# Optimization experiments

Measured on AMD Instinct MI355X. Metric: run time of the kernel, lower is better.

## Reference

```python
import jax, jax.numpy as jnp
import numpy as np
from jax import lax

B, L, C = 4, 4096, 512
H = 8           # head_num
D = C // H      # head dim = 64
RR = 4          # reduction_ratio -> reducer conv kernel 7, stride 4
KS = 3          # MixFFN depthwise kernel
ER = 4          # expansion ratio -> 2048 channels
EPS = 1e-5      # torch LayerNorm default eps


def _ln(x, g, b):
    # LayerNorm over last axis, affine per-channel
    m = jnp.mean(x, axis=-1, keepdims=True)
    v = jnp.mean(jnp.square(x - m), axis=-1, keepdims=True)
    return (x - m) * lax.rsqrt(v + EPS) * g + b


def setup_inputs() -> dict:
    key = jax.random.key(0)
    ks = jax.random.split(key, 9)
    s = lambda fan: 1.0 / np.sqrt(fan)
    return {
        "x": jax.random.normal(ks[0], (B, L, C), jnp.float32),
        "w_q": jax.random.normal(ks[1], (C, C), jnp.float32) * s(C),
        "w_k": jax.random.normal(ks[2], (C, C), jnp.float32) * s(C),
        "w_v": jax.random.normal(ks[3], (C, C), jnp.float32) * s(C),
        "w_o": jax.random.normal(ks[4], (C, C), jnp.float32) * s(C),
        "w_red": jax.random.normal(ks[5], (C, C, 2 * RR - 1), jnp.float32) * s(C * (2 * RR - 1)),
        "w_ffn1": jax.random.normal(ks[6], (C, C), jnp.float32) * s(C),
        "w_ffn_dw": jax.random.normal(ks[7], (C * ER, 1, KS), jnp.float32) * s(KS),
        "w_ffn2": jax.random.normal(ks[8], (C, C * ER), jnp.float32) * s(C * ER),
        "ln_gamma": jnp.ones((6, C), jnp.float32),
        "ln_beta": jnp.zeros((6, C), jnp.float32),
    }


def reference(x, w_q, w_k, w_v, w_o, w_red, w_ffn1, w_ffn_dw, w_ffn2, ln_gamma, ln_beta):
    # ln indices: 0=ln1(pre-attn), 1=ln(reducer), 2=ln_q, 3=ln_k, 4=ln_v, 5=ln2(pre-ffn)
    residual = x
    h = _ln(x, ln_gamma[0], ln_beta[0])  # B L C

    # --- spatial-reduction for K/V: reflect-pad strided conv + LN ---
    p = (2 * RR - 1) // 2
    hr = jnp.transpose(h, (0, 2, 1))  # B C L
    hr = jnp.pad(hr, ((0, 0), (0, 0), (p, p)), mode="reflect")
    red = lax.conv_general_dilated(hr, w_red, window_strides=(RR,), padding="VALID",
                                   dimension_numbers=("NCH", "OIH", "NCH"))  # B C Lr
    red = jnp.transpose(red, (0, 2, 1))  # B Lr C
    red = _ln(red, ln_gamma[1], ln_beta[1])

    # --- QKV projections + LayerNorms ---
    q = _ln(h @ w_q.T, ln_gamma[2], ln_beta[2])      # B L C
    k = _ln(red @ w_k.T, ln_gamma[3], ln_beta[3])    # B Lr C
    v = _ln(red @ w_v.T, ln_gamma[4], ln_beta[4])    # B Lr C

    Lr = k.shape[1]
    q = q.reshape(B, L, H, D).transpose(0, 2, 1, 3)   # B h L d
    k = k.reshape(B, Lr, H, D).transpose(0, 2, 1, 3)  # B h Lr d
    v = v.reshape(B, Lr, H, D).transpose(0, 2, 1, 3)

    scores = jnp.einsum("bhqd,bhkd->bhqk", q, k) / jnp.sqrt(jnp.float32(D))
    attn = jax.nn.softmax(scores, axis=-1)
    out = jnp.einsum("bhqk,bhkd->bhqd", attn, v)
    out = out.transpose(0, 2, 1, 3).reshape(B, L, C)
    out = out @ w_o.T

    h2 = out + residual
    residual2 = h2
    f = _ln(h2, ln_gamma[5], ln_beta[5])  # B L C

    # --- MixFFN: 1x1 conv -> depthwise reflect conv (groups=C, out=ER*C) -> GELU -> 1x1 conv ---
    f = jnp.transpose(f, (0, 2, 1))  # B C L
    f = jnp.einsum("oi,bil->bol", w_ffn1, f)  # 1x1, C->C
    pk = (KS - 1) // 2
    fp = jnp.pad(f, ((0, 0), (0, 0), (pk, pk)), mode="reflect")
    f = lax.conv_general_dilated(fp, w_ffn_dw, window_strides=(1,), padding="VALID",
                                 dimension_numbers=("NCH", "OIH", "NCH"),
                                 feature_group_count=C)  # B (ER*C) L
    f = jax.nn.gelu(f, approximate=False)  # torch nn.GELU() is exact erf
    f = jnp.einsum("oi,bil->bol", w_ffn2, f)  # 1x1, ER*C->C
    f = jnp.transpose(f, (0, 2, 1))  # B L C

    return f + residual2
```

## Files before the change

kernel.cpp:

```cpp
#include <hip/hip_runtime.h>
#include <math.h>

typedef __attribute__((ext_vector_type(8))) short short8;
typedef __attribute__((ext_vector_type(4))) short short4v;
typedef __attribute__((ext_vector_type(4))) float f32x4;
typedef unsigned short u16;
typedef unsigned int u32;
typedef unsigned long long u64;

namespace {
constexpr int kB = 4;
constexpr int kL = 4096;
constexpr int kC = 512;
constexpr int kH = 8;
constexpr int kLr = 1024;
constexpr int kCH = 2048;
constexpr int kKred = 3584;
constexpr float kEps = 1e-5f;
}

#if __has_builtin(__builtin_amdgcn_mfma_f32_16x16x16bf16_1k)
#define MFMA16X16(a, b, c) __builtin_amdgcn_mfma_f32_16x16x16bf16_1k((a), (b), (c), 0, 0, 0)
#else
__device__ __forceinline__ f32x4 mfma16_fb(short4v a, short4v b, f32x4 c) {
  asm volatile("v_mfma_f32_16x16x16_bf16 %0, %1, %2, %0\n\ts_nop 7\n\ts_nop 3"
               : "+v"(c) : "v"(a), "v"(b));
  return c;
}
#define MFMA16X16(a, b, c) mfma16_fb((a), (b), (c))
#endif

__device__ __forceinline__ float bf2f(u16 u) { return __uint_as_float(((u32)u) << 16); }
__device__ __forceinline__ u16 f2bf(float f) {
  u32 u = __float_as_uint(f);
  u32 r = (u + 0x7fffu + ((u >> 16) & 1u)) >> 16;
  return (u16)r;
}
__device__ __forceinline__ u32 cvtpk(float lo, float hi) {
  u32 r;
  asm("v_cvt_pk_bf16_f32 %0, %1, %2" : "=v"(r) : "v"(lo), "v"(hi));
  return r;
}
__device__ __forceinline__ float fexp2(float x) {
#if __has_builtin(__builtin_amdgcn_exp2f)
  return __builtin_amdgcn_exp2f(x);
#else
  float r;
  asm("v_exp_f32 %0, %1" : "=v"(r) : "v"(x));
  return r;
#endif
}

__device__ __forceinline__ void gload_lds16(const void* g, void* l) {
  __builtin_amdgcn_global_load_lds(
      (const __attribute__((address_space(1))) unsigned int*)g,
      (__attribute__((address_space(3))) unsigned int*)l, 16, 0, 0);
}

__device__ __forceinline__ short8 ldsfrag(const u16* base, int row, int col16) {
  return *(const short8*)(base + (size_t)(((row << 3) + (col16 ^ (row & 7))) << 3));
}

__global__ __launch_bounds__(256) void cvt_weights_kernel(
    const float* __restrict__ w_q, const float* __restrict__ w_k,
    const float* __restrict__ w_v, const float* __restrict__ w_o,
    const float* __restrict__ w_f1, const float* __restrict__ w_f2,
    u16* __restrict__ dst) {
  const int i = (blockIdx.x * 256 + threadIdx.x) * 4;
  const int seg = i >> 18;
  const float* src;
  int off;
  if (seg < 5) {
    src = (seg == 0) ? w_q : (seg == 1) ? w_k : (seg == 2) ? w_v : (seg == 3) ? w_o : w_f1;
    off = i & 262143;
  } else {
    src = w_f2;
    off = i - 1310720;
  }
  const float4 v = *(const float4*)(src + off);
  u16 o[4] = {f2bf(v.x), f2bf(v.y), f2bf(v.z), f2bf(v.w)};
  *(u64*)(dst + i) = *(u64*)o;
}

__global__ __launch_bounds__(256) void repack_wred_kernel(const float* __restrict__ src,
                                                          u16* __restrict__ dst) {
  const int idx = blockIdx.x * 256 + threadIdx.x;
  if (idx >= kC * kKred) return;
  const int o = idx / kKred;
  const int rem = idx - o * kKred;
  const int t = rem >> 9;
  const int i = rem & (kC - 1);
  dst[idx] = f2bf(src[(size_t)(o * kC + i) * 7 + t]);
}

__global__ __launch_bounds__(256) void ln_bf16_kernel(const float* __restrict__ in,
                                                      u16* __restrict__ out,
                                                      const float* __restrict__ g,
                                                      const float* __restrict__ be) {
  const int row = blockIdx.x;
  const int tid = threadIdx.x;
  const float2 v = *(const float2*)(in + (size_t)row * kC + tid * 2);
  float s = v.x + v.y;
  float ss = v.x * v.x + v.y * v.y;
#pragma unroll
  for (int off = 32; off > 0; off >>= 1) {
    s += __shfl_down(s, off);
    ss += __shfl_down(ss, off);
  }
  __shared__ float wsum[4][2];
  __shared__ float mi[2];
  const int wave = tid >> 6, lane = tid & 63;
  if (lane == 0) { wsum[wave][0] = s; wsum[wave][1] = ss; }
  __syncthreads();
  if (tid == 0) {
    const float S = wsum[0][0] + wsum[1][0] + wsum[2][0] + wsum[3][0];
    const float SS = wsum[0][1] + wsum[1][1] + wsum[2][1] + wsum[3][1];
    const float mean = S * (1.0f / kC);
    const float var = SS * (1.0f / kC) - mean * mean;
    mi[0] = mean;
    mi[1] = rsqrtf(var + kEps);
  }
  __syncthreads();
  const float mean = mi[0], inv = mi[1];
  const float2 gg = *(const float2*)(g + tid * 2);
  const float2 bb = *(const float2*)(be + tid * 2);
  u16 o2[2] = {f2bf((v.x - mean) * inv * gg.x + bb.x), f2bf((v.y - mean) * inv * gg.y + bb.y)};
  *(u32*)(out + (size_t)row * kC + tid * 2) = *(u32*)o2;
}

__global__ __launch_bounds__(256) void reduce2_ln_kernel(const float* __restrict__ P,
                                                         u16* __restrict__ out,
                                                         const float* __restrict__ g,
                                                         const float* __restrict__ be) {
  const int row = blockIdx.x;
  const int tid = threadIdx.x;
  const size_t stride = (size_t)kB * kLr * kC;
  float2 v = make_float2(0.f, 0.f);
#pragma unroll
  for (int z = 0; z < 2; ++z) {
    const float2 p = *(const float2*)(P + z * stride + (size_t)row * kC + tid * 2);
    v.x += p.x;
    v.y += p.y;
  }
  float s = v.x + v.y;
  float ss = v.x * v.x + v.y * v.y;
#pragma unroll
  for (int off = 32; off > 0; off >>= 1) {
    s += __shfl_down(s, off);
    ss += __shfl_down(ss, off);
  }
  __shared__ float wsum[4][2];
  __shared__ float mi[2];
  const int wave = tid >> 6, lane = tid & 63;
  if (lane == 0) { wsum[wave][0] = s; wsum[wave][1] = ss; }
  __syncthreads();
  if (tid == 0) {
    const float S = wsum[0][0] + wsum[1][0] + wsum[2][0] + wsum[3][0];
    const float SS = wsum[0][1] + wsum[1][1] + wsum[2][1] + wsum[3][1];
    const float mean = S * (1.0f / kC);
    const float var = SS * (1.0f / kC) - mean * mean;
    mi[0] = mean;
    mi[1] = rsqrtf(var + kEps);
  }
  __syncthreads();
  const float mean = mi[0], inv = mi[1];
  const float2 gg = *(const float2*)(g + tid * 2);
  const float2 bb = *(const float2*)(be + tid * 2);
  u16 o2[2] = {f2bf((v.x - mean) * inv * gg.x + bb.x), f2bf((v.y - mean) * inv * gg.y + bb.y)};
  *(u32*)(out + (size_t)row * kC + tid * 2) = *(u32*)o2;
}

__global__ __launch_bounds__(256) void dwgelu_kernel(const u16* __restrict__ f1,
                                                     const float* __restrict__ wdw,
                                                     u16* __restrict__ fdw) {
  const int row = blockIdx.x;
  const int l = row & (kL - 1);
  const int rb = row - l;
  const int cc0 = threadIdx.x * 8;
  const int cg = cc0 >> 2;
  const int lm = (l == 0) ? 1 : l - 1;
  const int lp = (l == kL - 1) ? kL - 2 : l + 1;
  const u32 xm = *(const u32*)(f1 + (size_t)(rb + lm) * kC + cg);
  const u32 x0 = *(const u32*)(f1 + (size_t)(rb + l) * kC + cg);
  const u32 xp = *(const u32*)(f1 + (size_t)(rb + lp) * kC + cg);
  const float xml = bf2f((u16)xm), xmh = bf2f((u16)(xm >> 16));
  const float x0l = bf2f((u16)x0), x0h = bf2f((u16)(x0 >> 16));
  const float xpl = bf2f((u16)xp), xph = bf2f((u16)(xp >> 16));
  float wv[24];
#pragma unroll
  for (int t = 0; t < 6; ++t)
    *(float4*)&wv[t * 4] = *(const float4*)(wdw + (size_t)cc0 * 3 + t * 4);
  short8 pk;
#pragma unroll
  for (int j = 0; j < 8; ++j) {
    const float a_ = (j < 4) ? xml : xmh;
    const float b_ = (j < 4) ? x0l : x0h;
    const float c_ = (j < 4) ? xpl : xph;
    const float dw = wv[j * 3] * a_ + wv[j * 3 + 1] * b_ + wv[j * 3 + 2] * c_;
    pk[j] = (short)f2bf(0.5f * dw * (1.0f + erff(dw * 0.70710678118654752440f)));
  }
  *(short8*)(fdw + (size_t)row * kCH + cc0) = pk;
}

__global__ __launch_bounds__(256) void mgemm_red_kernel(
    const u16* __restrict__ A, const u16* __restrict__ W, float* __restrict__ OutF,
    int M, int N, int K) {
  __shared__ __align__(16) u16 As[2][128 * 64];
  __shared__ __align__(16) u16 Bs[2][128 * 64];
  const int tid = threadIdx.x;
  const int lane = tid & 63, w = tid >> 6;
  const int bid = blockIdx.x;
  const int m0 = (bid & 31) << 7, n0 = (bid >> 5) << 7;
  const int wm = (w >> 1) * 64, wn = (w & 1) * 64;
  const f32x4 zero = {0.f, 0.f, 0.f, 0.f};
  f32x4 acc[4][4];
#pragma unroll
  for (int i = 0; i < 4; ++i)
#pragma unroll
    for (int j = 0; j < 4; ++j) acc[i][j] = zero;

  const int kc = K / gridDim.z;
  const int kBeg = blockIdx.z * kc;
  float* outp = OutF + (size_t)blockIdx.z * M * N;

  auto stage = [&](int buf, int k0) {
#pragma unroll
    for (int c = 0; c < 4; ++c) {
      const int ci = w * 4 + c;
      const int idx = ci * 64 + lane;
      const int row = idx >> 3, s = idx & 7;
      const int c16 = s ^ (row & 7);
      gload_lds16(W + (size_t)(n0 + row) * K + k0 + c16 * 8, (char*)Bs[buf] + ci * 1024);
      const int m = m0 + row;
      const int b = m >> 10, lr = m & (kLr - 1);
      const int k = k0 + c16 * 8;
      const int t = k >> 9, i = k & (kC - 1);
      int pos = 4 * lr + t - 3;
      pos = pos < 0 ? -pos : (pos >= kL ? 2 * kL - 2 - pos : pos);
      gload_lds16(A + ((size_t)(b << 12) + pos) * kC + i, (char*)As[buf] + ci * 1024);
    }
  };

  const int nk = kc >> 6;
  stage(0, kBeg);
  __syncthreads();
  for (int t = 0; t < nk; ++t) {
    const int cur = t & 1;
    if (t + 1 < nk) stage(cur ^ 1, kBeg + ((t + 1) << 6));
#pragma unroll
    for (int kst = 0; kst < 2; ++kst) {
      short8 af[4], bfr[4];
      const int c16 = kst * 4 + (lane >> 4);
#pragma unroll
      for (int mb = 0; mb < 4; ++mb) af[mb] = ldsfrag(As[cur], wm + mb * 16 + (lane & 15), c16);
#pragma unroll
      for (int nb = 0; nb < 4; ++nb) bfr[nb] = ldsfrag(Bs[cur], wn + nb * 16 + (lane & 15), c16);
#pragma unroll
      for (int mb = 0; mb < 4; ++mb)
#pragma unroll
        for (int nb = 0; nb < 4; ++nb)
          acc[mb][nb] = __builtin_amdgcn_mfma_f32_16x16x32_bf16(af[mb], bfr[nb], acc[mb][nb], 0, 0, 0);
    }
    __syncthreads();
  }
#pragma unroll
  for (int mb = 0; mb < 4; ++mb)
#pragma unroll
    for (int r = 0; r < 4; ++r) {
      const int row = m0 + wm + mb * 16 + ((lane >> 4) << 2) + r;
#pragma unroll
      for (int nb = 0; nb < 4; ++nb)
        outp[(size_t)row * N + n0 + wn + nb * 16 + (lane & 15)] = acc[mb][nb][r];
    }
}

__global__ __launch_bounds__(256) void mgemm_res_kernel(
    const u16* __restrict__ A, const u16* __restrict__ W,
    const float* __restrict__ Res, float* __restrict__ OutF, int M, int N, int K) {
  __shared__ __align__(16) u16 As[2][128 * 64];
  __shared__ __align__(16) u16 Bs[2][128 * 64];
  const int tid = threadIdx.x;
  const int lane = tid & 63, w = tid >> 6;
  const int bid = blockIdx.x;
  const int m0 = (bid & 127) << 7, n0 = (bid >> 7) << 7;
  const int wm = (w >> 1) * 64, wn = (w & 1) * 64;
  const f32x4 zero = {0.f, 0.f, 0.f, 0.f};
  f32x4 acc[4][4];
#pragma unroll
  for (int i = 0; i < 4; ++i)
#pragma unroll
    for (int j = 0; j < 4; ++j) acc[i][j] = zero;

  auto stage = [&](int buf, int k0) {
#pragma unroll
    for (int c = 0; c < 4; ++c) {
      const int ci = w * 4 + c;
      const int idx = ci * 64 + lane;
      const int row = idx >> 3, s = idx & 7;
      const int c16 = s ^ (row & 7);
      gload_lds16(W + (size_t)(n0 + row) * K + k0 + c16 * 8, (char*)Bs[buf] + ci * 1024);
      gload_lds16(A + (size_t)(m0 + row) * K + k0 + c16 * 8, (char*)As[buf] + ci * 1024);
    }
  };

  const int nk = K >> 6;
  stage(0, 0);
  __syncthreads();
  for (int t = 0; t < nk; ++t) {
    const int cur = t & 1;
    if (t + 1 < nk) stage(cur ^ 1, (t + 1) << 6);
#pragma unroll
    for (int kst = 0; kst < 2; ++kst) {
      short8 af[4], bfr[4];
      const int c16 = kst * 4 + (lane >> 4);
#pragma unroll
      for (int mb = 0; mb < 4; ++mb) af[mb] = ldsfrag(As[cur], wm + mb * 16 + (lane & 15), c16);
#pragma unroll
      for (int nb = 0; nb < 4; ++nb) bfr[nb] = ldsfrag(Bs[cur], wn + nb * 16 + (lane & 15), c16);
#pragma unroll
      for (int mb = 0; mb < 4; ++mb)
#pragma unroll
        for (int nb = 0; nb < 4; ++nb)
          acc[mb][nb] = __builtin_amdgcn_mfma_f32_16x16x32_bf16(af[mb], bfr[nb], acc[mb][nb], 0, 0, 0);
    }
    __syncthreads();
  }
#pragma unroll
  for (int mb = 0; mb < 4; ++mb)
#pragma unroll
    for (int r = 0; r < 4; ++r) {
      const int row = m0 + wm + mb * 16 + ((lane >> 4) << 2) + r;
#pragma unroll
      for (int nb = 0; nb < 4; ++nb) {
        const size_t off = (size_t)row * N + n0 + wn + nb * 16 + (lane & 15);
        OutF[off] = acc[mb][nb][r] + Res[off];
      }
    }
}

template <int EPI>
__global__ __launch_bounds__(1024) void gemm512_kernel(
    const u16* __restrict__ A, const u16* __restrict__ W,
    const float* __restrict__ Res, float* __restrict__ OutF,
    u16* __restrict__ OutB, u16* __restrict__ OutB2,
    int K, const float* __restrict__ gam, const float* __restrict__ bet, float oscale) {
  constexpr bool RES_ = (EPI == 3);
  constexpr bool LN_ = (EPI == 1 || EPI == 2 || EPI == 3);
  __shared__ __align__(16) u16 As[2][64 * 64];
  __shared__ __align__(16) u16 Bs[2][512 * 64];
  const int tid = threadIdx.x;
  const int lane = tid & 63, w = tid >> 6;
  const int l15 = lane & 15, g = lane >> 4;
  int bx, by;
  if (EPI == 2) { bx = blockIdx.x >> 6; by = blockIdx.x & 63; }
  else { bx = 0; by = blockIdx.x; }
  const int m0 = by * 64;
  const int n0 = bx * 512;
  const int wm = (w >> 3) << 5;
  const int wn = (w & 7) << 6;
  const f32x4 zero = {0.f, 0.f, 0.f, 0.f};
  f32x4 acc[2][4];
#pragma unroll
  for (int i = 0; i < 2; ++i)
#pragma unroll
    for (int j = 0; j < 4; ++j) acc[i][j] = zero;

  auto stage = [&](int buf, int k0) {
#pragma unroll
    for (int c = 0; c < 4; ++c) {
      const int cg = (w << 2) + c;
      const int idx = (cg << 6) + lane;
      const int row = idx >> 3, sl = idx & 7;
      const int c16 = sl ^ (row & 7);
      gload_lds16(W + (size_t)(n0 + row) * K + k0 + (c16 << 3), (char*)Bs[buf] + cg * 1024);
    }
    if (w < 8) {
      const int idx = (w << 6) + lane;
      const int row = idx >> 3, sl = idx & 7;
      const int c16 = sl ^ (row & 7);
      gload_lds16(A + (size_t)(m0 + row) * K + k0 + (c16 << 3), (char*)As[buf] + w * 1024);
    }
  };

  const int nk = K >> 6;
  stage(0, 0);
  __syncthreads();
  for (int t = 0; t < nk; ++t) {
    const int cur = t & 1;
    if (t + 1 < nk) stage(cur ^ 1, (t + 1) << 6);
#pragma unroll
    for (int kst = 0; kst < 2; ++kst) {
      const int c16 = (kst << 2) + g;
      short8 af[2], bfr[4];
#pragma unroll
      for (int mb = 0; mb < 2; ++mb) af[mb] = ldsfrag(As[cur], wm + (mb << 4) + l15, c16);
#pragma unroll
      for (int nb = 0; nb < 4; ++nb) bfr[nb] = ldsfrag(Bs[cur], wn + (nb << 4) + l15, c16);
#pragma unroll
      for (int mb = 0; mb < 2; ++mb)
#pragma unroll
        for (int nb = 0; nb < 4; ++nb)
          acc[mb][nb] = __builtin_amdgcn_mfma_f32_16x16x32_bf16(af[mb], bfr[nb], acc[mb][nb], 0, 0, 0);
    }
    __syncthreads();
  }

  if (RES_) {
#pragma unroll
    for (int mb = 0; mb < 2; ++mb)
#pragma unroll
      for (int r = 0; r < 4; ++r) {
        const int grow = m0 + wm + (mb << 4) + (g << 2) + r;
#pragma unroll
        for (int nb = 0; nb < 4; ++nb)
          acc[mb][nb][r] += Res[(size_t)grow * kC + wn + (nb << 4) + l15];
      }
  }
  float* rs = (float*)As[0];
  float* rs2 = rs + 512;
  float2* minv = (float2*)(rs2 + 512);
  if (LN_) {
#pragma unroll
    for (int mb = 0; mb < 2; ++mb)
#pragma unroll
      for (int r = 0; r < 4; ++r) {
        float s = acc[mb][0][r] + acc[mb][1][r] + acc[mb][2][r] + acc[mb][3][r];
        float s2 = acc[mb][0][r] * acc[mb][0][r] + acc[mb][1][r] * acc[mb][1][r] +
                   acc[mb][2][r] * acc[mb][2][r] + acc[mb][3][r] * acc[mb][3][r];
        s += __shfl_xor(s, 1); s += __shfl_xor(s, 2); s += __shfl_xor(s, 4); s += __shfl_xor(s, 8);
        s2 += __shfl_xor(s2, 1); s2 += __shfl_xor(s2, 2); s2 += __shfl_xor(s2, 4); s2 += __shfl_xor(s2, 8);
        if (l15 == 0) {
          const int rowf = wm + (mb << 4) + (g << 2) + r;
          rs[((w & 7) << 6) + rowf] = s;
          rs2[((w & 7) << 6) + rowf] = s2;
        }
      }
    __syncthreads();
    if (tid < 64) {
      float S = 0.f, SS = 0.f;
#pragma unroll
      for (int c8 = 0; c8 < 8; ++c8) { S += rs[(c8 << 6) + tid]; SS += rs2[(c8 << 6) + tid]; }
      const float mean = S * (1.0f / 512.0f);
      const float var = SS * (1.0f / 512.0f) - mean * mean;
      minv[tid] = make_float2(mean, rsqrtf(var + kEps));
    }
    __syncthreads();
  }
  float g4[4], b4[4];
  if (LN_) {
    const float* gp = (EPI == 2 && bx) ? gam + kC : gam;
    const float* bp = (EPI == 2 && bx) ? bet + kC : bet;
#pragma unroll
    for (int nb = 0; nb < 4; ++nb) {
      const int cc = wn + (nb << 4) + l15;
      g4[nb] = gp[cc];
      b4[nb] = bp[cc];
    }
  }
#pragma unroll
  for (int mb = 0; mb < 2; ++mb) {
#pragma unroll
    for (int r = 0; r < 4; ++r) {
      const int rowf = wm + (mb << 4) + (g << 2) + r;
      const int grow = m0 + rowf;
      float2 mi = make_float2(0.f, 0.f);
      if (LN_) mi = minv[rowf];
#pragma unroll
      for (int nb = 0; nb < 4; ++nb) {
        const int cc = wn + (nb << 4) + l15;
        const float vv = acc[mb][nb][r];
        if (EPI == 0) {
          OutB[(size_t)grow * kC + cc] = f2bf(vv);
        } else if (EPI == 1) {
          OutB[(size_t)grow * kC + cc] = f2bf(((vv - mi.x) * mi.y * g4[nb] + b4[nb]) * oscale);
        } else if (EPI == 2) {
          const float lv = (vv - mi.x) * mi.y * g4[nb] + b4[nb];
          if (bx == 0) {
            OutB[(size_t)grow * kC + cc] = f2bf(lv);
          } else {
            const int b = grow >> 10, lr = grow & (kLr - 1);
            const int hh = cc >> 6, d = cc & 63;
            OutB2[((size_t)((b << 3) + hh) * 64 + d) * kLr + lr] = f2bf(lv);
          }
        } else {
          OutF[(size_t)grow * kC + cc] = vv;
          OutB[(size_t)grow * kC + cc] = f2bf((vv - mi.x) * mi.y * g4[nb] + b4[nb]);
        }
      }
    }
  }
}

__global__ __launch_bounds__(512, 4) void attn_mfma_kernel(
    const u16* __restrict__ q, const u16* __restrict__ k,
    const u16* __restrict__ vt, u16* __restrict__ o) {
  __shared__ __align__(16) u16 Ks[2][128 * 64];
  __shared__ __align__(16) char Vp[2][64 * 264];
  const int tid = threadIdx.x;
  const int lane = tid & 63, w = tid >> 6;
  const int bid = blockIdx.x;
  const int qt = bid >> 5;
  const int hb = bid & 31;
  const int h = hb >> 2, b = hb & 3;
  const int q0 = qt << 7;
  const int l15 = lane & 15, g = lane >> 4;

  short8 qf[2];
#pragma unroll
  for (int kst = 0; kst < 2; ++kst)
    qf[kst] = *(const short8*)(q + (size_t)((b << 12) + q0 + (w << 4) + l15) * kC +
                               (h << 6) + kst * 32 + g * 8);

  int kbase[2];
#pragma unroll
  for (int kst = 0; kst < 2; ++kst)
    kbase[kst] = (l15 << 7) + (((((kst << 2) + g) ^ (l15 & 7))) << 4);
  int voff[8];
#pragma unroll
  for (int nb = 0; nb < 8; ++nb) {
    const int chunk = (nb << 1) + (g >> 1);
    const int slot = chunk ^ (l15 & 7);
    voff[nb] = l15 * 264 + (slot << 4) + ((g & 1) << 3);
  }

  const int r_ = tid >> 3;
  const int sl_ = tid & 7;
  const int c16 = sl_ ^ (r_ & 7);
  const u16* kSrc = k + (size_t)((b << 10) + r_) * kC + (h << 6) + (c16 << 3);
  const u16* vSrc = vt + (size_t)(((b << 3) + h) * 64 + r_) * kLr + (c16 << 3);
  const int vdoff = r_ * 264 + (sl_ << 4);

  auto stageK = [&](int buf) {
    gload_lds16(kSrc, (char*)Ks[buf] + tid * 16);
    gload_lds16(kSrc + (size_t)64 * kC, (char*)Ks[buf] + 8192 + tid * 16);
  };

  stageK(0);
  kSrc += (size_t)128 * kC;
  {
    const float4 v0 = *(const float4*)vSrc;
    const float4 v1 = *(const float4*)(vSrc + 64);
    vSrc += 128;
    char* vd = Vp[0] + vdoff;
    *(float2*)(vd) = make_float2(v0.x, v0.y);
    *(float2*)(vd + 8) = make_float2(v0.z, v0.w);
    *(float2*)(vd + 128) = make_float2(v1.x, v1.y);
    *(float2*)(vd + 136) = make_float2(v1.z, v1.w);
  }

  const f32x4 zero = {0.f, 0.f, 0.f, 0.f};
  float l1 = 0.f;
  f32x4 accO[4] = {zero, zero, zero, zero};
  constexpr int nt = kLr / 128;

  __syncthreads();

  for (int t = 0; t < nt; ++t) {
    const int cur = t & 1;
    float4 vn0, vn1;
    if (t + 1 < nt) {
      vn0 = *(const float4*)vSrc;
      vn1 = *(const float4*)(vSrc + 64);
      vSrc += 128;
      stageK(cur ^ 1);
      kSrc += (size_t)128 * kC;
    }
    const char* kb = (const char*)Ks[cur];
    f32x4 st[8];
#pragma unroll
    for (int nb = 0; nb < 8; ++nb) st[nb] = zero;
    __builtin_amdgcn_s_setprio(1);
#pragma unroll
    for (int kst = 0; kst < 2; ++kst)
#pragma unroll
      for (int nb = 0; nb < 8; ++nb) {
        const short8 ak = *(const short8*)(kb + (nb << 11) + kbase[kst]);
        st[nb] = __builtin_amdgcn_mfma_f32_16x16x32_bf16(ak, qf[kst], st[nb], 0, 0, 0);
      }
    __builtin_amdgcn_s_setprio(0);
    short4v pa[8];
    {
      float ps = 0.f;
#pragma unroll
      for (int nb = 0; nb < 8; ++nb) {
#pragma unroll
        for (int r = 0; r < 4; ++r) {
          const float e = fexp2(st[nb][r]);
          st[nb][r] = e;
          ps += e;
        }
        u32 pw[2];
        pw[0] = cvtpk(st[nb][0], st[nb][1]);
        pw[1] = cvtpk(st[nb][2], st[nb][3]);
        pa[nb] = *(short4v*)pw;
      }
      l1 += ps;
    }
    const char* vbuf = Vp[cur];
    __builtin_amdgcn_s_setprio(1);
#pragma unroll
    for (int nb = 0; nb < 8; ++nb) {
#pragma unroll
      for (int d = 0; d < 4; ++d) {
        const short4v vb = *(const short4v*)(vbuf + voff[nb] + d * 4224);
        accO[d] = MFMA16X16(pa[nb], vb, accO[d]);
      }
    }
    __builtin_amdgcn_s_setprio(0);
    if (t + 1 < nt) {
      char* vd = Vp[cur ^ 1] + vdoff;
      *(float2*)(vd) = make_float2(vn0.x, vn0.y);
      *(float2*)(vd + 8) = make_float2(vn0.z, vn0.w);
      *(float2*)(vd + 128) = make_float2(vn1.x, vn1.y);
      *(float2*)(vd + 136) = make_float2(vn1.z, vn1.w);
    }
    __syncthreads();
  }
  l1 += __shfl_xor(l1, 16);
  l1 += __shfl_xor(l1, 32);
  float li[4];
#pragma unroll
  for (int r = 0; r < 4; ++r) li[r] = 1.0f / __shfl(l1, (g << 2) + r);
  const int qg = (b << 12) + q0 + (w << 4) + (g << 2);
#pragma unroll
  for (int d = 0; d < 4; ++d)
#pragma unroll
    for (int r = 0; r < 4; ++r)
      o[(size_t)(qg + r) * kC + (h << 6) + (d << 4) + l15] = f2bf(accO[d][r] * li[r]);
}

extern "C" void kernel_launch(void* const* d_in, const int* in_sizes, int n_in,
                              void* d_out, int out_size, void* d_ws, size_t ws_size,
                              hipStream_t stream) {
  const float* x      = (const float*)d_in[0];
  const float* w_q    = (const float*)d_in[1];
  const float* w_k    = (const float*)d_in[2];
  const float* w_v    = (const float*)d_in[3];
  const float* w_o    = (const float*)d_in[4];
  const float* w_red  = (const float*)d_in[5];
  const float* w_ffn1 = (const float*)d_in[6];
  const float* w_dw   = (const float*)d_in[7];
  const float* w_ffn2 = (const float*)d_in[8];
  const float* gam    = (const float*)d_in[9];
  const float* bet    = (const float*)d_in[10];
  float* out = (float*)d_out;

  const size_t nBLC = (size_t)kB * kL * kC;
  const size_t nBLrC = (size_t)kB * kLr * kC;
  u16* us = (u16*)d_ws;
  u16* wqb   = us;
  u16* wkb   = wqb + 262144;
  u16* wob   = wkb + 2 * 262144;
  u16* wf1b  = wob + 262144;
  u16* wf2b  = wf1b + 262144;
  u16* wredb = wf2b + 1048576;
  u16* h_b   = wredb + 1835008;
  u16* q_b   = h_b + nBLC;
  u16* red_b = q_b + nBLC;
  u16* k_b   = red_b + nBLrC;
  u16* vt_b  = k_b + nBLrC;
  float* S   = (float*)(vt_b + nBLrC);
  u16* fdw   = q_b;

  cvt_weights_kernel<<<2304, 256, 0, stream>>>(w_q, w_k, w_v, w_o, w_ffn1, w_ffn2, wqb);
  repack_wred_kernel<<<7168, 256, 0, stream>>>(w_red, wredb);

  ln_bf16_kernel<<<kB * kL, 256, 0, stream>>>(x, h_b, gam, bet);
  mgemm_red_kernel<<<dim3(128, 1, 2), 256, 0, stream>>>(h_b, wredb, S, kB * kLr, kC, kKred);
  reduce2_ln_kernel<<<kB * kLr, 256, 0, stream>>>(S, red_b, gam + kC, bet + kC);
  gemm512_kernel<1><<<dim3(256), 1024, 0, stream>>>(
      h_b, wqb, nullptr, nullptr, q_b, nullptr, kC, gam + 2 * kC, bet + 2 * kC,
      0.125f * 1.44269504088896f);
  gemm512_kernel<2><<<dim3(128), 1024, 0, stream>>>(
      red_b, wkb, nullptr, nullptr, k_b, vt_b, kC, gam + 3 * kC, bet + 3 * kC, 1.0f);
  attn_mfma_kernel<<<dim3(1024), 512, 0, stream>>>(q_b, k_b, vt_b, h_b);
  gemm512_kernel<3><<<dim3(256), 1024, 0, stream>>>(
      h_b, wob, x, out, q_b, nullptr, kC, gam + 5 * kC, bet + 5 * kC, 1.0f);
  gemm512_kernel<0><<<dim3(256), 1024, 0, stream>>>(
      q_b, wf1b, nullptr, nullptr, h_b, nullptr, kC, nullptr, nullptr, 1.0f);
  dwgelu_kernel<<<kB * kL, 256, 0, stream>>>(h_b, w_dw, fdw);
  mgemm_res_kernel<<<dim3(512), 256, 0, stream>>>(fdw, wf2b, out, out, kB * kL, kC, kCH);
}
```

Baseline: 273.2 us.

## Process two query sub-tiles per wave in attention to reuse K/V LDS fragments

The attention kernel now runs 256 threads per block instead of 512. Each wave handles 32 query rows as two 16-row sub-tiles, and each K and V fragment read from LDS feeds two MFMAs. This halves LDS reads per MFMA and the number of waves doing staging, so each thread now loads more K/V data per tile. The cost is doubled accumulator and score registers per wave (st[2][8], accO[2][4]) and fewer waves for hiding latency.

```diff
diff --git a/kernel.cpp b/kernel.cpp
--- a/kernel.cpp
+++ b/kernel.cpp
@@ -491,7 +491,7 @@
   }
 }
 
-__global__ __launch_bounds__(512, 4) void attn_mfma_kernel(
+__global__ __launch_bounds__(256, 2) void attn_mfma_kernel(
     const u16* __restrict__ q, const u16* __restrict__ k,
     const u16* __restrict__ vt, u16* __restrict__ o) {
   __shared__ __align__(16) u16 Ks[2][128 * 64];
@@ -505,11 +505,13 @@
   const int q0 = qt << 7;
   const int l15 = lane & 15, g = lane >> 4;
 
-  short8 qf[2];
-#pragma unroll
-  for (int kst = 0; kst < 2; ++kst)
-    qf[kst] = *(const short8*)(q + (size_t)((b << 12) + q0 + (w << 4) + l15) * kC +
-                               (h << 6) + kst * 32 + g * 8);
+  short8 qf[2][2];
+#pragma unroll
+  for (int s = 0; s < 2; ++s)
+#pragma unroll
+    for (int kst = 0; kst < 2; ++kst)
+      qf[s][kst] = *(const short8*)(q + (size_t)((b << 12) + q0 + (w << 5) + (s << 4) + l15) * kC +
+                                    (h << 6) + kst * 32 + g * 8);
 
   int kbase[2];
 #pragma unroll
@@ -523,78 +525,101 @@
     voff[nb] = l15 * 264 + (slot << 4) + ((g & 1) << 3);
   }
 
-  const int r_ = tid >> 3;
-  const int sl_ = tid & 7;
-  const int c16 = sl_ ^ (r_ & 7);
-  const u16* kSrc = k + (size_t)((b << 10) + r_) * kC + (h << 6) + (c16 << 3);
-  const u16* vSrc = vt + (size_t)(((b << 3) + h) * 64 + r_) * kLr + (c16 << 3);
-  const int vdoff = r_ * 264 + (sl_ << 4);
+  const int kr_ = tid >> 3;
+  const int ksl_ = tid & 7;
+  const int kc16 = ksl_ ^ (kr_ & 7);
+  const u16* kSrc = k + (size_t)((b << 10) + kr_) * kC + (h << 6) + (kc16 << 3);
+  const int rv_ = tid >> 2;
+  const int jv_ = tid & 3;
+  const int vc16a = jv_ ^ (rv_ & 7);
+  const int vc16b = (jv_ + 4) ^ (rv_ & 7);
+  const u16* vSrc = vt + (size_t)(((b << 3) + h) * 64 + rv_) * kLr;
+  const int vdoff = rv_ * 264 + (jv_ << 4);
 
   auto stageK = [&](int buf) {
-    gload_lds16(kSrc, (char*)Ks[buf] + tid * 16);
-    gload_lds16(kSrc + (size_t)64 * kC, (char*)Ks[buf] + 8192 + tid * 16);
+#pragma unroll
+    for (int c = 0; c < 4; ++c)
+      gload_lds16(kSrc + (size_t)(c << 5) * kC, (char*)Ks[buf] + (c << 12) + (tid << 4));
+  };
+  auto loadV = [&](int kv0, float4* vn) {
+    vn[0] = *(const float4*)(vSrc + kv0 + (vc16a << 3));
+    vn[1] = *(const float4*)(vSrc + kv0 + (vc16b << 3));
+    vn[2] = *(const float4*)(vSrc + kv0 + 64 + (vc16a << 3));
+    vn[3] = *(const float4*)(vSrc + kv0 + 64 + (vc16b << 3));
+  };
+  auto writeV = [&](int buf, const float4* vn) {
+    char* vd = Vp[buf] + vdoff;
+    *(float2*)(vd) = make_float2(vn[0].x, vn[0].y);
+    *(float2*)(vd + 8) = make_float2(vn[0].z, vn[0].w);
+    *(float2*)(vd + 64) = make_float2(vn[1].x, vn[1].y);
+    *(float2*)(vd + 72) = make_float2(vn[1].z, vn[1].w);
+    *(float2*)(vd + 128) = make_float2(vn[2].x, vn[2].y);
+    *(float2*)(vd + 136) = make_float2(vn[2].z, vn[2].w);
+    *(float2*)(vd + 192) = make_float2(vn[3].x, vn[3].y);
+    *(float2*)(vd + 200) = make_float2(vn[3].z, vn[3].w);
   };
 
   stageK(0);
   kSrc += (size_t)128 * kC;
   {
-    const float4 v0 = *(const float4*)vSrc;
-    const float4 v1 = *(const float4*)(vSrc + 64);
-    vSrc += 128;
-    char* vd = Vp[0] + vdoff;
-    *(float2*)(vd) = make_float2(v0.x, v0.y);
-    *(float2*)(vd + 8) = make_float2(v0.z, v0.w);
-    *(float2*)(vd + 128) = make_float2(v1.x, v1.y);
-    *(float2*)(vd + 136) = make_float2(v1.z, v1.w);
+    float4 v0[4];
+    loadV(0, v0);
+    writeV(0, v0);
   }
 
   const f32x4 zero = {0.f, 0.f, 0.f, 0.f};
-  float l1 = 0.f;
-  f32x4 accO[4] = {zero, zero, zero, zero};
+  float l1[2] = {0.f, 0.f};
+  f32x4 accO[2][4];
+#pragma unroll
+  for (int s = 0; s < 2; ++s)
+#pragma unroll
+    for (int d = 0; d < 4; ++d) accO[s][d] = zero;
   constexpr int nt = kLr / 128;
 
   __syncthreads();
 
   for (int t = 0; t < nt; ++t) {
     const int cur = t & 1;
-    float4 vn0, vn1;
+    float4 vn[4];
     if (t + 1 < nt) {
-      vn0 = *(const float4*)vSrc;
-      vn1 = *(const float4*)(vSrc + 64);
-      vSrc += 128;
+      loadV((t + 1) << 7, vn);
       stageK(cur ^ 1);
       kSrc += (size_t)128 * kC;
     }
     const char* kb = (const char*)Ks[cur];
-    f32x4 st[8];
-#pragma unroll
-    for (int nb = 0; nb < 8; ++nb) st[nb] = zero;
+    f32x4 st[2][8];
+#pragma unroll
+    for (int s = 0; s < 2; ++s)
+#pragma unroll
+      for (int nb = 0; nb < 8; ++nb) st[s][nb] = zero;
     __builtin_amdgcn_s_setprio(1);
 #pragma unroll
     for (int kst = 0; kst < 2; ++kst)
 #pragma unroll
       for (int nb = 0; nb < 8; ++nb) {
         const short8 ak = *(const short8*)(kb + (nb << 11) + kbase[kst]);
-        st[nb] = __builtin_amdgcn_mfma_f32_16x16x32_bf16(ak, qf[kst], st[nb], 0, 0, 0);
+        st[0][nb] = __builtin_amdgcn_mfma_f32_16x16x32_bf16(ak, qf[0][kst], st[0][nb], 0, 0, 0);
+        st[1][nb] = __builtin_amdgcn_mfma_f32_16x16x32_bf16(ak, qf[1][kst], st[1][nb], 0, 0, 0);
       }
     __builtin_amdgcn_s_setprio(0);
-    short4v pa[8];
-    {
+    short4v pa[2][8];
+#pragma unroll
+    for (int s = 0; s < 2; ++s) {
       float ps = 0.f;
 #pragma unroll
       for (int nb = 0; nb < 8; ++nb) {
 #pragma unroll
         for (int r = 0; r < 4; ++r) {
-          const float e = fexp2(st[nb][r]);
-          st[nb][r] = e;
+          const float e = fexp2(st[s][nb][r]);
+          st[s][nb][r] = e;
           ps += e;
         }
         u32 pw[2];
-        pw[0] = cvtpk(st[nb][0], st[nb][1]);
-        pw[1] = cvtpk(st[nb][2], st[nb][3]);
-        pa[nb] = *(short4v*)pw;
+        pw[0] = cvtpk(st[s][nb][0], st[s][nb][1]);
+        pw[1] = cvtpk(st[s][nb][2], st[s][nb][3]);
+        pa[s][nb] = *(short4v*)pw;
       }
-      l1 += ps;
+      l1[s] += ps;
     }
     const char* vbuf = Vp[cur];
     __builtin_amdgcn_s_setprio(1);
@@ -603,30 +628,28 @@
 #pragma unroll
       for (int d = 0; d < 4; ++d) {
         const short4v vb = *(const short4v*)(vbuf + voff[nb] + d * 4224);
-        accO[d] = MFMA16X16(pa[nb], vb, accO[d]);
+        accO[0][d] = MFMA16X16(pa[0][nb], vb, accO[0][d]);
+        accO[1][d] = MFMA16X16(pa[1][nb], vb, accO[1][d]);
       }
     }
     __builtin_amdgcn_s_setprio(0);
-    if (t + 1 < nt) {
-      char* vd = Vp[cur ^ 1] + vdoff;
-      *(float2*)(vd) = make_float2(vn0.x, vn0.y);
-      *(float2*)(vd + 8) = make_float2(vn0.z, vn0.w);
-      *(float2*)(vd + 128) = make_float2(vn1.x, vn1.y);
-      *(float2*)(vd + 136) = make_float2(vn1.z, vn1.w);
-    }
+    if (t + 1 < nt) writeV(cur ^ 1, vn);
     __syncthreads();
   }
-  l1 += __shfl_xor(l1, 16);
-  l1 += __shfl_xor(l1, 32);
-  float li[4];
-#pragma unroll
-  for (int r = 0; r < 4; ++r) li[r] = 1.0f / __shfl(l1, (g << 2) + r);
-  const int qg = (b << 12) + q0 + (w << 4) + (g << 2);
-#pragma unroll
-  for (int d = 0; d < 4; ++d)
-#pragma unroll
-    for (int r = 0; r < 4; ++r)
-      o[(size_t)(qg + r) * kC + (h << 6) + (d << 4) + l15] = f2bf(accO[d][r] * li[r]);
+#pragma unroll
+  for (int s = 0; s < 2; ++s) {
+    l1[s] += __shfl_xor(l1[s], 16);
+    l1[s] += __shfl_xor(l1[s], 32);
+    float li[4];
+#pragma unroll
+    for (int r = 0; r < 4; ++r) li[r] = 1.0f / __shfl(l1[s], (g << 2) + r);
+    const int qg = (b << 12) + q0 + (w << 5) + (s << 4) + (g << 2);
+#pragma unroll
+    for (int d = 0; d < 4; ++d)
+#pragma unroll
+      for (int r = 0; r < 4; ++r)
+        o[(size_t)(qg + r) * kC + (h << 6) + (d << 4) + l15] = f2bf(accO[s][d][r] * li[r]);
+  }
 }
 
 extern "C" void kernel_launch(void* const* d_in, const int* in_sizes, int n_in,
@@ -673,7 +696,7 @@
       0.125f * 1.44269504088896f);
   gemm512_kernel<2><<<dim3(128), 1024, 0, stream>>>(
       red_b, wkb, nullptr, nullptr, k_b, vt_b, kC, gam + 3 * kC, bet + 3 * kC, 1.0f);
-  attn_mfma_kernel<<<dim3(1024), 512, 0, stream>>>(q_b, k_b, vt_b, h_b);
+  attn_mfma_kernel<<<dim3(1024), 256, 0, stream>>>(q_b, k_b, vt_b, h_b);
   gemm512_kernel<3><<<dim3(256), 1024, 0, stream>>>(
       h_b, wob, x, out, q_b, nullptr, kC, gam + 5 * kC, bet + 5 * kC, 1.0f);
   gemm512_kernel<0><<<dim3(256), 1024, 0, stream>>>(
```

Measured after the change: 275.5 us. No clear change (+0.9%).

## Process two 16-row query subtiles per wave in attention kernel

Applied to the files above, without the earlier changes.

Each wave now handles 32 query rows instead of 16, so each block covers 256 queries and the grid is halved to 512 blocks. Every K and V fragment loaded from LDS feeds two MFMAs, which halves LDS reads and global K/V staging per query. The cost is roughly twice the accumulator and score registers, which could hurt occupancy under the 512-thread launch bound. Fewer blocks also means less parallelism to fill the machine.

```diff
diff --git a/kernel.cpp b/kernel.cpp
--- a/kernel.cpp
+++ b/kernel.cpp
@@ -502,14 +502,16 @@
   const int qt = bid >> 5;
   const int hb = bid & 31;
   const int h = hb >> 2, b = hb & 3;
-  const int q0 = qt << 7;
+  const int q0 = qt << 8;
   const int l15 = lane & 15, g = lane >> 4;
 
-  short8 qf[2];
-#pragma unroll
-  for (int kst = 0; kst < 2; ++kst)
-    qf[kst] = *(const short8*)(q + (size_t)((b << 12) + q0 + (w << 4) + l15) * kC +
-                               (h << 6) + kst * 32 + g * 8);
+  short8 qf[2][2];
+#pragma unroll
+  for (int s = 0; s < 2; ++s)
+#pragma unroll
+    for (int kst = 0; kst < 2; ++kst)
+      qf[s][kst] = *(const short8*)(q + (size_t)((b << 12) + q0 + (w << 5) + (s << 4) + l15) * kC +
+                                    (h << 6) + kst * 32 + g * 8);
 
   int kbase[2];
 #pragma unroll
@@ -549,8 +551,12 @@
   }
 
   const f32x4 zero = {0.f, 0.f, 0.f, 0.f};
-  float l1 = 0.f;
-  f32x4 accO[4] = {zero, zero, zero, zero};
+  float l1[2] = {0.f, 0.f};
+  f32x4 accO[2][4];
+#pragma unroll
+  for (int s = 0; s < 2; ++s)
+#pragma unroll
+    for (int d = 0; d < 4; ++d) accO[s][d] = zero;
   constexpr int nt = kLr / 128;
 
   __syncthreads();
@@ -566,35 +572,39 @@
       kSrc += (size_t)128 * kC;
     }
     const char* kb = (const char*)Ks[cur];
-    f32x4 st[8];
-#pragma unroll
-    for (int nb = 0; nb < 8; ++nb) st[nb] = zero;
+    f32x4 st[2][8];
+#pragma unroll
+    for (int s = 0; s < 2; ++s)
+#pragma unroll
+      for (int nb = 0; nb < 8; ++nb) st[s][nb] = zero;
     __builtin_amdgcn_s_setprio(1);
 #pragma unroll
     for (int kst = 0; kst < 2; ++kst)
 #pragma unroll
       for (int nb = 0; nb < 8; ++nb) {
         const short8 ak = *(const short8*)(kb + (nb << 11) + kbase[kst]);
-        st[nb] = __builtin_amdgcn_mfma_f32_16x16x32_bf16(ak, qf[kst], st[nb], 0, 0, 0);
+        st[0][nb] = __builtin_amdgcn_mfma_f32_16x16x32_bf16(ak, qf[0][kst], st[0][nb], 0, 0, 0);
+        st[1][nb] = __builtin_amdgcn_mfma_f32_16x16x32_bf16(ak, qf[1][kst], st[1][nb], 0, 0, 0);
       }
     __builtin_amdgcn_s_setprio(0);
-    short4v pa[8];
-    {
+    short4v pa[2][8];
+#pragma unroll
+    for (int s = 0; s < 2; ++s) {
       float ps = 0.f;
 #pragma unroll
       for (int nb = 0; nb < 8; ++nb) {
 #pragma unroll
         for (int r = 0; r < 4; ++r) {
-          const float e = fexp2(st[nb][r]);
-          st[nb][r] = e;
+          const float e = fexp2(st[s][nb][r]);
+          st[s][nb][r] = e;
           ps += e;
         }
         u32 pw[2];
-        pw[0] = cvtpk(st[nb][0], st[nb][1]);
-        pw[1] = cvtpk(st[nb][2], st[nb][3]);
-        pa[nb] = *(short4v*)pw;
+        pw[0] = cvtpk(st[s][nb][0], st[s][nb][1]);
+        pw[1] = cvtpk(st[s][nb][2], st[s][nb][3]);
+        pa[s][nb] = *(short4v*)pw;
       }
-      l1 += ps;
+      l1[s] += ps;
     }
     const char* vbuf = Vp[cur];
     __builtin_amdgcn_s_setprio(1);
@@ -603,7 +613,8 @@
 #pragma unroll
       for (int d = 0; d < 4; ++d) {
         const short4v vb = *(const short4v*)(vbuf + voff[nb] + d * 4224);
-        accO[d] = MFMA16X16(pa[nb], vb, accO[d]);
+        accO[0][d] = MFMA16X16(pa[0][nb], vb, accO[0][d]);
+        accO[1][d] = MFMA16X16(pa[1][nb], vb, accO[1][d]);
       }
     }
     __builtin_amdgcn_s_setprio(0);
@@ -616,17 +627,20 @@
     }
     __syncthreads();
   }
-  l1 += __shfl_xor(l1, 16);
-  l1 += __shfl_xor(l1, 32);
-  float li[4];
-#pragma unroll
-  for (int r = 0; r < 4; ++r) li[r] = 1.0f / __shfl(l1, (g << 2) + r);
-  const int qg = (b << 12) + q0 + (w << 4) + (g << 2);
-#pragma unroll
-  for (int d = 0; d < 4; ++d)
-#pragma unroll
-    for (int r = 0; r < 4; ++r)
-      o[(size_t)(qg + r) * kC + (h << 6) + (d << 4) + l15] = f2bf(accO[d][r] * li[r]);
+#pragma unroll
+  for (int s = 0; s < 2; ++s) {
+    l1[s] += __shfl_xor(l1[s], 16);
+    l1[s] += __shfl_xor(l1[s], 32);
+    float li[4];
+#pragma unroll
+    for (int r = 0; r < 4; ++r) li[r] = 1.0f / __shfl(l1[s], (g << 2) + r);
+    const int qg = (b << 12) + q0 + (w << 5) + (s << 4) + (g << 2);
+#pragma unroll
+    for (int d = 0; d < 4; ++d)
+#pragma unroll
+      for (int r = 0; r < 4; ++r)
+        o[(size_t)(qg + r) * kC + (h << 6) + (d << 4) + l15] = f2bf(accO[s][d][r] * li[r]);
+  }
 }
 
 extern "C" void kernel_launch(void* const* d_in, const int* in_sizes, int n_in,
@@ -673,7 +687,7 @@
       0.125f * 1.44269504088896f);
   gemm512_kernel<2><<<dim3(128), 1024, 0, stream>>>(
       red_b, wkb, nullptr, nullptr, k_b, vt_b, kC, gam + 3 * kC, bet + 3 * kC, 1.0f);
-  attn_mfma_kernel<<<dim3(1024), 512, 0, stream>>>(q_b, k_b, vt_b, h_b);
+  attn_mfma_kernel<<<dim3(512), 512, 0, stream>>>(q_b, k_b, vt_b, h_b);
   gemm512_kernel<3><<<dim3(256), 1024, 0, stream>>>(
       h_b, wob, x, out, q_b, nullptr, kC, gam + 5 * kC, bet + 5 * kC, 1.0f);
   gemm512_kernel<0><<<dim3(256), 1024, 0, stream>>>(
```

Measured after the change: 404.1 us. +47.9%, slower.
